# Performance work log

Measured on AMD Instinct MI355X. Metric: run time of the kernel, lower is better.

The kernel has to match this reference:

```python
import jax, jax.numpy as jnp
import numpy as np

B, S, D = 4, 2048, 512
H, HD = 8, 64            # n_heads, head_dim = D // H
E, K, F = 8, 2, 1024     # n_experts, top_k, d_ff
EPS = 1e-6


def setup_inputs() -> dict:
    key = jax.random.key(0)
    ks = jax.random.split(key, 16)
    sd = 0.02
    return {
        "inputs": jax.random.normal(ks[0], (B, S, D), jnp.float32),
        "rms1_w": jnp.ones((D,), jnp.float32),
        "wq": jax.random.normal(ks[1], (D, H, HD), jnp.float32) * sd,
        "bq": jnp.zeros((H, HD), jnp.float32),
        "wk": jax.random.normal(ks[2], (D, H, HD), jnp.float32) * sd,
        "bk": jnp.zeros((H, HD), jnp.float32),
        "wv": jax.random.normal(ks[3], (D, H, HD), jnp.float32) * sd,
        "bv": jnp.zeros((H, HD), jnp.float32),
        "wo": jax.random.normal(ks[4], (H, HD, D), jnp.float32) * sd,
        "bo": jnp.zeros((D,), jnp.float32),
        "rms2_w": jnp.ones((D,), jnp.float32),
        "gate_w": jax.random.normal(ks[5], (D, E), jnp.float32) * sd,
        "ew1": jax.random.normal(ks[6], (E, D, F), jnp.float32) * sd,
        "eb1": jnp.zeros((E, F), jnp.float32),
        "ew2": jax.random.normal(ks[7], (E, F, D), jnp.float32) * sd,
        "eb2": jnp.zeros((E, D), jnp.float32),
    }


def _rmsnorm(x, w):
    return x * jax.lax.rsqrt(jnp.mean(x * x, axis=-1, keepdims=True) + EPS) * w


def _mha(x, wq, bq, wk, bk, wv, bv, wo, bo):
    q = jnp.einsum("bsd,dhe->bshe", x, wq) + bq
    k = jnp.einsum("bsd,dhe->bshe", x, wk) + bk
    v = jnp.einsum("bsd,dhe->bshe", x, wv) + bv
    scores = jnp.einsum("bqhe,bkhe->bhqk", q, k) / jnp.sqrt(jnp.float32(HD))
    attn = jax.nn.softmax(scores, axis=-1)
    ctx = jnp.einsum("bhqk,bkhe->bqhe", attn, v)
    return jnp.einsum("bqhe,hed->bqd", ctx, wo) + bo


def _moe(x, gate_w, ew1, eb1, ew2, eb2):
    T = B * S
    xt = x.reshape(T, D)
    probs = jax.nn.softmax(xt @ gate_w, axis=-1)          # [T, E]
    topv, topi = jax.lax.top_k(probs, K)                   # [T, K]
    topv = topv / jnp.sum(topv, axis=-1, keepdims=True)    # renormalize
    # dense combine weights [T, E]
    wmat = jnp.sum(jax.nn.one_hot(topi, E, dtype=xt.dtype) * topv[..., None], axis=1)
    h = jax.nn.relu(jnp.einsum("td,edf->tef", xt, ew1) + eb1)   # [T, E, F]
    y = jnp.einsum("tef,efd->ted", h, ew2) + eb2                # [T, E, D]
    out = jnp.einsum("te,ted->td", wmat, y)
    return out.reshape(B, S, D)


def reference(inputs, rms1_w, wq, bq, wk, bk, wv, bv, wo, bo, rms2_w, gate_w, ew1, eb1, ew2, eb2):
    x = _rmsnorm(inputs, rms1_w)
    x = _mha(x, wq, bq, wk, bk, wv, bv, wo, bo)
    x1 = x + inputs
    x = _rmsnorm(x1, rms2_w)
    x = _moe(x, gate_w, ew1, eb1, ew2, eb2)
    # dropout is identity at inference
    return x + x1
```

## Files before the change

### kernel.cpp

```cpp
#include <hip/hip_runtime.h>
#include <hip/hip_bf16.h>

typedef unsigned short u16;
typedef __attribute__((ext_vector_type(8))) short short8;
typedef __attribute__((ext_vector_type(4))) short bf16x4;
typedef __attribute__((ext_vector_type(4))) float f32x4;
typedef __attribute__((ext_vector_type(4))) int i32x4;
typedef __attribute__((ext_vector_type(2))) unsigned u32x2;

#define DEV __device__ __forceinline__

DEV float bf2f(u16 v){ unsigned u = ((unsigned)v)<<16; float f; __builtin_memcpy(&f,&u,4); return f; }
DEV u16 f2bf(float f){ unsigned u; __builtin_memcpy(&u,&f,4); u += 0x7fff + ((u>>16)&1); return (u16)(u>>16); }

DEV void gload16(const void* g, void* l){
  __builtin_amdgcn_global_load_lds((const __attribute__((address_space(1))) void*)g,
                                   (__attribute__((address_space(3))) void*)l, 16, 0, 0);
}


__global__ __launch_bounds__(256) void k_tconv(const float* __restrict__ src, u16* __restrict__ dst,
    int R, int C){
  src += (size_t)blockIdx.z * R * C;
  dst += (size_t)blockIdx.z * R * C;
  int r0 = blockIdx.y * 64, c0 = blockIdx.x * 64;
  __shared__ u16 tile[64][68];
  int tid = threadIdx.x;
  int rr = tid >> 4, cc = (tid & 15) * 4;
  #pragma unroll
  for (int it = 0; it < 4; ++it){
    int r = it*16 + rr;
    float4 v = *(const float4*)(src + (size_t)(r0 + r)*C + c0 + cc);
    bf16x4 pk = { (short)f2bf(v.x), (short)f2bf(v.y), (short)f2bf(v.z), (short)f2bf(v.w) };
    *(bf16x4*)&tile[r][cc] = pk;
  }
  __syncthreads();
  #pragma unroll
  for (int it = 0; it < 4; ++it){
    int c = it*16 + rr;
    bf16x4 pk = { (short)tile[cc+0][c], (short)tile[cc+1][c],
                  (short)tile[cc+2][c], (short)tile[cc+3][c] };
    *(bf16x4*)(dst + (size_t)(c0 + c)*R + r0 + cc) = pk;
  }
}

__global__ __launch_bounds__(256) void k_vtrans(const u16* __restrict__ src, u16* __restrict__ dst){
  int bh = blockIdx.y; int s0 = blockIdx.x*64;
  src += (size_t)bh*2048*64 + (size_t)s0*64;
  dst += (size_t)bh*64*2048 + s0;
  __shared__ unsigned tile[64*33];
  int tid = threadIdx.x;
  #pragma unroll
  for (int it = 0; it < 2; ++it){
    int c = tid + it*256;
    int r = c >> 3, c8 = c & 7;
    i32x4 v = *(const i32x4*)(src + (size_t)r*64 + c8*8);
    *(i32x4*)&tile[r*33 + c8*4] = v;
  }
  __syncthreads();
  #pragma unroll
  for (int it = 0; it < 2; ++it){
    int c = tid + it*256;
    int d = c >> 3, s8 = c & 7;
    union { i32x4 v; u16 us[8]; } o;
    #pragma unroll
    for (int j = 0; j < 8; ++j){
      unsigned w = tile[(s8*8+j)*33 + (d>>1)];
      o.us[j] = (d & 1) ? (u16)(w >> 16) : (u16)(w & 0xffff);
    }
    *(i32x4*)(dst + (size_t)d*2048 + s8*8) = o.v;
  }
}

__global__ __launch_bounds__(256) void k_rmsnorm(const float* __restrict__ x, const float* __restrict__ w,
    u16* __restrict__ ob){
  int t = blockIdx.x, tid = threadIdx.x;
  const float* xr = x + (size_t)t*512;
  float2 v = *(const float2*)(xr + tid*2);
  float ss = v.x*v.x + v.y*v.y;
  #pragma unroll
  for (int o=32; o>0; o>>=1) ss += __shfl_down(ss, o);
  __shared__ float sred[4];
  if ((tid&63)==0) sred[tid>>6] = ss;
  __syncthreads();
  float tot = sred[0]+sred[1]+sred[2]+sred[3];
  float inv = rsqrtf(tot*(1.f/512.f) + 1e-6f);
  float2 wv = *(const float2*)(w + tid*2);
  ob[(size_t)t*512 + tid*2]     = f2bf(v.x*inv*wv.x);
  ob[(size_t)t*512 + tid*2 + 1] = f2bf(v.y*inv*wv.y);
}

__global__ __launch_bounds__(256) void k_rmsgate(const float* __restrict__ x, const float* __restrict__ w,
    const float* __restrict__ gw, u16* __restrict__ ob, int* __restrict__ topi, float* __restrict__ topw){
  int t = blockIdx.x, tid = threadIdx.x;
  const float* xr = x + (size_t)t*512;
  float2 v = *(const float2*)(xr + tid*2);
  float ss = v.x*v.x + v.y*v.y;
  #pragma unroll
  for (int o=32; o>0; o>>=1) ss += __shfl_down(ss, o);
  __shared__ float sred[4];
  if ((tid&63)==0) sred[tid>>6] = ss;
  __syncthreads();
  float tot = sred[0]+sred[1]+sred[2]+sred[3];
  float inv = rsqrtf(tot*(1.f/512.f) + 1e-6f);
  float2 wv = *(const float2*)(w + tid*2);
  float y0 = v.x*inv*wv.x, y1 = v.y*inv*wv.y;
  ob[(size_t)t*512 + tid*2]     = f2bf(y0);
  ob[(size_t)t*512 + tid*2 + 1] = f2bf(y1);
  float acc[8];
  const float* g0 = gw + tid*16;
  #pragma unroll
  for (int e=0;e<8;e++) acc[e] = y0*g0[e] + y1*g0[8+e];
  #pragma unroll
  for (int dd=1; dd<64; dd<<=1)
    #pragma unroll
    for (int e=0;e<8;e++) acc[e] += __shfl_xor(acc[e], dd);
  __shared__ float gred[4][8];
  if ((tid&63)==0)
    #pragma unroll
    for (int e=0;e<8;e++) gred[tid>>6][e] = acc[e];
  __syncthreads();
  if (tid==0){
    float l[8];
    #pragma unroll
    for (int e=0;e<8;e++) l[e] = gred[0][e]+gred[1][e]+gred[2][e]+gred[3][e];
    int i0=0; float a0=l[0];
    #pragma unroll
    for (int e=1;e<8;e++) if (l[e]>a0){ a0=l[e]; i0=e; }
    int i1=-1; float a1=-1e30f;
    #pragma unroll
    for (int e=0;e<8;e++) if (e!=i0 && l[e]>a1){ a1=l[e]; i1=e; }
    float w1 = __expf(a1 - a0);
    float invs = 1.f / (1.f + w1);
    topi[t*2]=i0; topi[t*2+1]=i1;
    topw[t*2]=invs; topw[t*2+1]=w1*invs;
  }
}

__global__ __launch_bounds__(256) void k_count(const int* __restrict__ topi, int* __restrict__ counts){
  __shared__ int lcnt[8];
  if (threadIdx.x < 8) lcnt[threadIdx.x] = 0;
  __syncthreads();
  for (int i = blockIdx.x*256 + threadIdx.x; i < 16384; i += 256*64)
    atomicAdd(&lcnt[topi[i]], 1);
  __syncthreads();
  if (threadIdx.x < 8) atomicAdd(&counts[threadIdx.x], lcnt[threadIdx.x]);
}

template<int MODE>
__global__ __launch_bounds__(256) void k_gemm(const u16* __restrict__ A, const u16* __restrict__ Bt,
    int Nsize, int Ksize,
    const float* __restrict__ b0, const float* __restrict__ b1, const float* __restrict__ b2,
    const float* __restrict__ resid, float* __restrict__ outf,
    u16* __restrict__ o0, u16* __restrict__ o1, u16* __restrict__ o2,
    const int* __restrict__ ebase, const int* __restrict__ ecnt, const int* __restrict__ etok)
{
  int nNT = Nsize >> 7;
  int e=0, mt, nt, myBase=0, myCnt=0;
  if constexpr (MODE>=2){
    int per = 128*nNT;
    e = blockIdx.x / per;
    int rr = blockIdx.x - e*per;
    mt = rr / nNT; nt = rr - mt*nNT;
    myCnt = ecnt[e]; myBase = ebase[e];
    if (mt*128 >= myCnt) return;
    Bt += (size_t)e * Nsize * Ksize;
  } else {
    mt = blockIdx.x / nNT; nt = blockIdx.x - mt*nNT;
  }
  __shared__ u16 As[128*32];
  __shared__ u16 Bs[128*32];
  int tid = threadIdx.x;
  int lane = tid & 63, wid = tid >> 6;
  int wr = (wid>>1)<<6, wc = (wid&1)<<6;
  int lrow = lane & 15, lk8 = (lane>>4)<<3;
  const u16* asrc[2]; const u16* bsrc[2];
  u16* aldst[2]; u16* bldst[2];
  #pragma unroll
  for (int it=0; it<2; ++it){
    int c = it*256 + tid;
    int r = c >> 2, c4 = c & 3;
    int grow;
    if constexpr (MODE==2){
      int ml = mt*128 + r; if (ml >= myCnt) ml = myCnt-1;
      grow = etok[myBase + ml];
    } else if constexpr (MODE==3){
      int ml = mt*128 + r; if (ml >= myCnt) ml = myCnt-1;
      grow = myBase + ml;
    } else {
      grow = mt*128 + r;
    }
    asrc[it] = A + (size_t)grow*Ksize + c4*8;
    bsrc[it] = Bt + (size_t)(nt*128 + r)*Ksize + c4*8;
    aldst[it] = As + (it*256 + wid*64)*8;
    bldst[it] = Bs + (it*256 + wid*64)*8;
  }
  f32x4 acc[4][4] = {};
  int nK = Ksize >> 5;
  for (int ks = 0; ks < nK; ++ks){
    int k0 = ks<<5;
    #pragma unroll
    for (int it=0; it<2; ++it){
      gload16(asrc[it] + k0, aldst[it]);
      gload16(bsrc[it] + k0, bldst[it]);
    }
    __syncthreads();
    short8 a[4], b[4];
    #pragma unroll
    for (int i=0;i<4;i++) a[i] = *(const short8*)(As + (wr + i*16 + lrow)*32 + lk8);
    #pragma unroll
    for (int j=0;j<4;j++) b[j] = *(const short8*)(Bs + (wc + j*16 + lrow)*32 + lk8);
    #pragma unroll
    for (int i=0;i<4;i++)
      #pragma unroll
      for (int j=0;j<4;j++)
        acc[i][j] = __builtin_amdgcn_mfma_f32_16x16x32_bf16(a[i], b[j], acc[i][j], 0,0,0);
    __syncthreads();
  }
  #pragma unroll
  for (int i=0;i<4;i++){
    #pragma unroll
    for (int r=0;r<4;r++){
      int rowl = mt*128 + wr + i*16 + ((lane>>4)<<2) + r;
      #pragma unroll
      for (int j=0;j<4;j++){
        int col = nt*128 + wc + j*16 + lrow;
        float v = acc[i][j][r];
        if constexpr (MODE==0){
          int which = col >> 9; int hc = col & 511;
          const float* bias = which==0 ? b0 : (which==1 ? b1 : b2);
          v += bias[hc];
          if (which == 0) v *= 0.18033688011112042f;
          u16* dst = which==0 ? o0 : (which==1 ? o1 : o2);
          int bidx = rowl >> 11, s = rowl & 2047;
          int h = hc >> 6, hd = hc & 63;
          dst[((size_t)(bidx*8+h)*2048 + s)*64 + hd] = f2bf(v);
        } else if constexpr (MODE==1){
          v += b0[col] + resid[(size_t)rowl*512 + col];
          outf[(size_t)rowl*512 + col] = v;
        } else if constexpr (MODE==2){
          if (rowl < myCnt){
            v += b0[e*1024 + col];
            v = fmaxf(v, 0.f);
            o0[(size_t)(myBase+rowl)*1024 + col] = f2bf(v);
          }
        } else {
          if (rowl < myCnt){
            v += b0[e*512 + col];
            o0[(size_t)(myBase+rowl)*512 + col] = f2bf(v);
          }
        }
      }
    }
  }
}

__global__ __launch_bounds__(256) void k_attn(const u16* __restrict__ qb, const u16* __restrict__ kb,
    const u16* __restrict__ vtb, u16* __restrict__ ctx)
{
  int qt = blockIdx.x & 15;
  int bh = blockIdx.x >> 4;
  int b = bh >> 3, h = bh & 7;
  const size_t bho = (size_t)bh * (2048*64);
  int tid = threadIdx.x, lane = tid & 63, wid = tid >> 6;
  int lrow = lane & 15, g = lane >> 4;
  __shared__ u16 Ks[128*64];
  __shared__ u16 Vts[64*128];
  __shared__ u16 Ps[4][32*128];
  char* Ksb = (char*)Ks;
  char* Vsb = (char*)Vts;
  char* Psb = (char*)&Ps[wid][0];
  int q0 = qt*128 + wid*32;
  short8 qf[2][2];
  #pragma unroll
  for (int mm=0;mm<2;mm++)
    #pragma unroll
    for (int kf=0;kf<2;kf++)
      qf[mm][kf] = *(const short8*)(qb + bho + (size_t)(q0 + mm*16 + lrow)*64 + kf*32 + g*8);
  f32x4 oacc[2][4] = {};
  float lpart[2] = {0.f, 0.f};
  const int swz = (lrow & 7) << 4;

  size_t ksrc[4], vsrc[4];
  int kdst[4], vdst[4];
  #pragma unroll
  for (int it=0; it<4; ++it){
    int c = tid + it*256;
    int kr = c >> 3, kc8 = c & 7;
    ksrc[it] = bho + (size_t)kr*64 + kc8*8;
    kdst[it] = kr*128 + ((kc8*16) ^ ((kr&7)<<4));
    int vr = c >> 4, vc16 = c & 15;
    vsrc[it] = bho + (size_t)vr*2048 + vc16*8;
    vdst[it] = vr*256 + ((vc16*16) ^ ((vr&7)<<4));
  }
  i32x4 kreg[4], vreg[4];
  #pragma unroll
  for (int it=0; it<4; ++it){
    kreg[it] = *(const i32x4*)(kb + ksrc[it]);
    vreg[it] = *(const i32x4*)(vtb + vsrc[it]);
  }
  #pragma unroll
  for (int it=0; it<4; ++it){
    *(i32x4*)(Ksb + kdst[it]) = kreg[it];
    *(i32x4*)(Vsb + vdst[it]) = vreg[it];
  }
  __syncthreads();

  for (int kt=0; kt<16; ++kt){
    if (kt < 15){
      int k0 = (kt+1)*128;
      #pragma unroll
      for (int it=0; it<4; ++it){
        kreg[it] = *(const i32x4*)(kb + ksrc[it] + (size_t)k0*64);
        vreg[it] = *(const i32x4*)(vtb + vsrc[it] + k0);
      }
    }
    __builtin_amdgcn_s_setprio(1);
    #pragma unroll
    for (int nf=0; nf<8; ++nf){
      short8 kf0 = *(const short8*)(Ksb + (nf*16+lrow)*128 + ((g*16) ^ swz));
      short8 kf1 = *(const short8*)(Ksb + (nf*16+lrow)*128 + ((64 + g*16) ^ swz));
      #pragma unroll
      for (int mm=0; mm<2; ++mm){
        f32x4 s = {};
        s = __builtin_amdgcn_mfma_f32_16x16x32_bf16(kf0, qf[mm][0], s, 0,0,0);
        s = __builtin_amdgcn_mfma_f32_16x16x32_bf16(kf1, qf[mm][1], s, 0,0,0);
        float p0 = __builtin_amdgcn_exp2f(s[0]);
        float p1 = __builtin_amdgcn_exp2f(s[1]);
        float p2 = __builtin_amdgcn_exp2f(s[2]);
        float p3 = __builtin_amdgcn_exp2f(s[3]);
        lpart[mm] += (p0+p1)+(p2+p3);
        unsigned w0 = (unsigned)f2bf(p0) | ((unsigned)f2bf(p1)<<16);
        unsigned w1 = (unsigned)f2bf(p2) | ((unsigned)f2bf(p3)<<16);
        *(u32x2*)(Psb + (mm*16+lrow)*256 + ((nf*32 + g*8) ^ swz)) = (u32x2){w0, w1};
      }
    }
    short8 pfr[2][4];
    #pragma unroll
    for (int mm=0;mm<2;mm++)
      #pragma unroll
      for (int kf=0;kf<4;kf++)
        pfr[mm][kf] = *(const short8*)(Psb + (mm*16+lrow)*256 + ((kf*64 + g*16) ^ swz));
    #pragma unroll
    for (int dn=0;dn<4;dn++){
      #pragma unroll
      for (int kf=0;kf<4;kf++){
        short8 vf = *(const short8*)(Vsb + (dn*16+lrow)*256 + ((kf*64 + g*16) ^ swz));
        #pragma unroll
        for (int mm=0;mm<2;mm++)
          oacc[mm][dn] = __builtin_amdgcn_mfma_f32_16x16x32_bf16(pfr[mm][kf], vf, oacc[mm][dn], 0,0,0);
      }
    }
    __builtin_amdgcn_s_setprio(0);
    __syncthreads();
    if (kt < 15){
      #pragma unroll
      for (int it=0; it<4; ++it){
        *(i32x4*)(Ksb + kdst[it]) = kreg[it];
        *(i32x4*)(Vsb + vdst[it]) = vreg[it];
      }
      __syncthreads();
    }
  }
  float linv[2][4];
  #pragma unroll
  for (int mm=0;mm<2;mm++){
    float ls = lpart[mm];
    ls += __shfl_xor(ls, 16);
    ls += __shfl_xor(ls, 32);
    #pragma unroll
    for (int r=0;r<4;r++)
      linv[mm][r] = 1.0f / __shfl(ls, g*4 + r);
  }
  #pragma unroll
  for (int mm=0;mm<2;mm++){
    #pragma unroll
    for (int r=0;r<4;r++){
      int qrow = q0 + mm*16 + g*4 + r;
      #pragma unroll
      for (int dn=0;dn<4;dn++)
        ctx[((size_t)(b*2048 + qrow))*512 + h*64 + dn*16 + lrow] = f2bf(oacc[mm][dn][r] * linv[mm][r]);
    }
  }
}

__global__ void k_scan(const int* __restrict__ counts, int* __restrict__ base, int* __restrict__ cur){
  if (threadIdx.x==0 && blockIdx.x==0){
    int s=0;
    for (int e=0;e<8;e++){ base[e]=s; cur[e]=s; s+=counts[e]; }
  }
}

__global__ __launch_bounds__(256) void k_assign(const int* __restrict__ topi,
    int* __restrict__ cur, int* __restrict__ rowof, int* __restrict__ tokof)
{
  __shared__ int lcnt[8];
  __shared__ int gbase[8];
  int tid = threadIdx.x;
  if (tid < 8) lcnt[tid] = 0;
  __syncthreads();
  int t = blockIdx.x*256 + tid;
  int e0 = topi[t*2], e1 = topi[t*2+1];
  int r0 = atomicAdd(&lcnt[e0], 1);
  int r1 = atomicAdd(&lcnt[e1], 1);
  __syncthreads();
  if (tid < 8) gbase[tid] = atomicAdd(&cur[tid], lcnt[tid]);
  __syncthreads();
  int row0 = gbase[e0] + r0, row1 = gbase[e1] + r1;
  rowof[t*2]   = row0;  rowof[t*2+1] = row1;
  tokof[row0] = t;      tokof[row1] = t;
}

__global__ __launch_bounds__(256) void k_combine(const float* __restrict__ x1, const u16* __restrict__ y,
    const int* __restrict__ rowof, const float* __restrict__ topw, float* __restrict__ out)
{
  int t = blockIdx.x;
  int d0 = threadIdx.x*2;
  int r0 = rowof[t*2], r1 = rowof[t*2+1];
  float w0 = topw[t*2], w1 = topw[t*2+1];
  size_t o = (size_t)t*512 + d0;
  out[o]   = x1[o]   + w0*bf2f(y[(size_t)r0*512+d0])   + w1*bf2f(y[(size_t)r1*512+d0]);
  out[o+1] = x1[o+1] + w0*bf2f(y[(size_t)r0*512+d0+1]) + w1*bf2f(y[(size_t)r1*512+d0+1]);
}

extern "C" void kernel_launch(void* const* d_in, const int* in_sizes, int n_in,
                              void* d_out, int out_size, void* d_ws, size_t ws_size,
                              hipStream_t stream)
{
  const float* inputs = (const float*)d_in[0];
  const float* rms1_w = (const float*)d_in[1];
  const float* wq  = (const float*)d_in[2];
  const float* bq  = (const float*)d_in[3];
  const float* wk  = (const float*)d_in[4];
  const float* bk  = (const float*)d_in[5];
  const float* wv  = (const float*)d_in[6];
  const float* bv  = (const float*)d_in[7];
  const float* wo  = (const float*)d_in[8];
  const float* bo  = (const float*)d_in[9];
  const float* rms2_w = (const float*)d_in[10];
  const float* gate_w = (const float*)d_in[11];
  const float* ew1 = (const float*)d_in[12];
  const float* eb1 = (const float*)d_in[13];
  const float* ew2 = (const float*)d_in[14];
  const float* eb2 = (const float*)d_in[15];
  char* ws = (char*)d_ws;

  size_t off = 0;
  u16* WQKV = (u16*)(ws + off); off += 1536ull*512*2;
  u16* WOT  = (u16*)(ws + off); off += 512ull*512*2;
  u16* E1T  = (u16*)(ws + off); off += 8ull*1024*512*2;
  u16* E2T  = (u16*)(ws + off); off += 8ull*512*1024*2;
  u16* XN   = (u16*)(ws + off); u16* Hbuf = XN;      off += 8192ull*512*2;
  u16* Qb   = (u16*)(ws + off); off += 4ull*8*2048*64*2;
  u16* Kb   = (u16*)(ws + off); off += 4ull*8*2048*64*2;
  u16* Vb   = (u16*)(ws + off); off += 4ull*8*2048*64*2;
  u16* CTX  = (u16*)(ws + off); u16* Yb = CTX;       off += 8192ull*512*2;
  float* XN2F = (float*)(ws + off); u16* VbT = (u16*)XN2F; off += 8192ull*512*4;
  float* X1   = (float*)(ws + off); off += 8192ull*512*4;
  u16* XN2B   = (u16*)(ws + off); off += 8192ull*512*2;
  int*   TOPI = (int*)(ws + off); off += 16384*4;
  float* TOPW = (float*)(ws + off); off += 16384*4;
  int*  ROWOF = (int*)(ws + off); off += 16384*4;
  int*  TOKOF = (int*)(ws + off); off += 16384*4;
  int*  CNT   = (int*)(ws + off); off += 64;
  int*  BASE  = (int*)(ws + off); off += 64;
  int*  CUR   = (int*)(ws + off); off += 64;
  if (ws_size < off) return;
  (void)XN2F;

  k_tconv<<<dim3(8,8,1),   256, 0, stream>>>(wq, WQKV,              512, 512);
  k_tconv<<<dim3(8,8,1),   256, 0, stream>>>(wk, WQKV + 512*512,    512, 512);
  k_tconv<<<dim3(8,8,1),   256, 0, stream>>>(wv, WQKV + 2*512*512,  512, 512);
  k_tconv<<<dim3(8,8,1),   256, 0, stream>>>(wo, WOT,               512, 512);
  k_tconv<<<dim3(16,8,8),  256, 0, stream>>>(ew1, E1T,              512, 1024);
  k_tconv<<<dim3(8,16,8),  256, 0, stream>>>(ew2, E2T,              1024, 512);

  k_rmsnorm<<<8192, 256, 0, stream>>>(inputs, rms1_w, XN);

  k_gemm<0><<<64*12, 256, 0, stream>>>(XN, WQKV, 1536, 512, bq, bk, bv,
      nullptr, nullptr, Qb, Kb, Vb, nullptr, nullptr, nullptr);

  k_vtrans<<<dim3(32,32), 256, 0, stream>>>(Vb, VbT);

  k_attn<<<512, 256, 0, stream>>>(Qb, Kb, VbT, CTX);

  k_gemm<1><<<64*4, 256, 0, stream>>>(CTX, WOT, 512, 512, bo, nullptr, nullptr,
      inputs, X1, nullptr, nullptr, nullptr, nullptr, nullptr, nullptr);

  k_rmsgate<<<8192, 256, 0, stream>>>(X1, rms2_w, gate_w, XN2B, TOPI, TOPW);

  hipMemsetAsync(CNT, 0, 192, stream);
  k_count<<<64, 256, 0, stream>>>(TOPI, CNT);
  k_scan<<<1, 64, 0, stream>>>(CNT, BASE, CUR);
  k_assign<<<32, 256, 0, stream>>>(TOPI, CUR, ROWOF, TOKOF);

  k_gemm<2><<<8*128*8, 256, 0, stream>>>(XN2B, E1T, 1024, 512, eb1, nullptr, nullptr,
      nullptr, nullptr, Hbuf, nullptr, nullptr, BASE, CNT, TOKOF);
  k_gemm<3><<<8*128*4, 256, 0, stream>>>(Hbuf, E2T, 512, 1024, eb2, nullptr, nullptr,
      nullptr, nullptr, Yb, nullptr, nullptr, BASE, CNT, TOKOF);

  k_combine<<<8192, 256, 0, stream>>>(X1, Yb, ROWOF, TOPW, (float*)d_out);
}
```

Before: 269.9 us.

## Double-buffer GEMM LDS tiles and halve attention query tile per block

The bf16 GEMM now uses two LDS buffers for the A and B tiles. It prefetches the next K-slice with global_load_lds while the current slice feeds the MFMAs, removing the load-then-barrier stall at the top of each iteration. The attention kernel drops from 128 to 64 query rows per block, 16 per wave, which doubles the grid to 1024 blocks and shrinks the per-wave P scratch and accumulators. This trades more K/V reloads from global memory for more parallelism and lower register and LDS pressure per block. The GEMM doubles its LDS footprint, which may reduce occupancy.

Result: slower. 275.5 us (+2.1%).

```diff
diff --git a/kernel.cpp b/kernel.cpp
--- a/kernel.cpp
+++ b/kernel.cpp
@@ -168,14 +168,14 @@
   } else {
     mt = blockIdx.x / nNT; nt = blockIdx.x - mt*nNT;
   }
-  __shared__ u16 As[128*32];
-  __shared__ u16 Bs[128*32];
+  __shared__ u16 As[2][128*32];
+  __shared__ u16 Bs[2][128*32];
   int tid = threadIdx.x;
   int lane = tid & 63, wid = tid >> 6;
   int wr = (wid>>1)<<6, wc = (wid&1)<<6;
   int lrow = lane & 15, lk8 = (lane>>4)<<3;
   const u16* asrc[2]; const u16* bsrc[2];
-  u16* aldst[2]; u16* bldst[2];
+  int ldoff[2];
   #pragma unroll
   for (int it=0; it<2; ++it){
     int c = it*256 + tid;
@@ -192,24 +192,31 @@
     }
     asrc[it] = A + (size_t)grow*Ksize + c4*8;
     bsrc[it] = Bt + (size_t)(nt*128 + r)*Ksize + c4*8;
-    aldst[it] = As + (it*256 + wid*64)*8;
-    bldst[it] = Bs + (it*256 + wid*64)*8;
+    ldoff[it] = (it*256 + wid*64)*8;
   }
   f32x4 acc[4][4] = {};
   int nK = Ksize >> 5;
+  #pragma unroll
+  for (int it=0; it<2; ++it){
+    gload16(asrc[it], &As[0][ldoff[it]]);
+    gload16(bsrc[it], &Bs[0][ldoff[it]]);
+  }
+  __syncthreads();
   for (int ks = 0; ks < nK; ++ks){
-    int k0 = ks<<5;
-    #pragma unroll
-    for (int it=0; it<2; ++it){
-      gload16(asrc[it] + k0, aldst[it]);
-      gload16(bsrc[it] + k0, bldst[it]);
-    }
-    __syncthreads();
+    int cur = ks & 1;
+    if (ks+1 < nK){
+      int k0 = (ks+1) << 5;
+      #pragma unroll
+      for (int it=0; it<2; ++it){
+        gload16(asrc[it] + k0, &As[cur^1][ldoff[it]]);
+        gload16(bsrc[it] + k0, &Bs[cur^1][ldoff[it]]);
+      }
+    }
     short8 a[4], b[4];
     #pragma unroll
-    for (int i=0;i<4;i++) a[i] = *(const short8*)(As + (wr + i*16 + lrow)*32 + lk8);
-    #pragma unroll
-    for (int j=0;j<4;j++) b[j] = *(const short8*)(Bs + (wc + j*16 + lrow)*32 + lk8);
+    for (int i=0;i<4;i++) a[i] = *(const short8*)(&As[cur][(wr + i*16 + lrow)*32 + lk8]);
+    #pragma unroll
+    for (int j=0;j<4;j++) b[j] = *(const short8*)(&Bs[cur][(wc + j*16 + lrow)*32 + lk8]);
     #pragma unroll
     for (int i=0;i<4;i++)
       #pragma unroll
@@ -258,27 +265,25 @@
 __global__ __launch_bounds__(256) void k_attn(const u16* __restrict__ qb, const u16* __restrict__ kb,
     const u16* __restrict__ vtb, u16* __restrict__ ctx)
 {
-  int qt = blockIdx.x & 15;
-  int bh = blockIdx.x >> 4;
+  int qt = blockIdx.x & 31;
+  int bh = blockIdx.x >> 5;
   int b = bh >> 3, h = bh & 7;
   const size_t bho = (size_t)bh * (2048*64);
   int tid = threadIdx.x, lane = tid & 63, wid = tid >> 6;
   int lrow = lane & 15, g = lane >> 4;
   __shared__ u16 Ks[128*64];
   __shared__ u16 Vts[64*128];
-  __shared__ u16 Ps[4][32*128];
+  __shared__ u16 Ps[4][16*64];
   char* Ksb = (char*)Ks;
   char* Vsb = (char*)Vts;
   char* Psb = (char*)&Ps[wid][0];
-  int q0 = qt*128 + wid*32;
-  short8 qf[2][2];
-  #pragma unroll
-  for (int mm=0;mm<2;mm++)
-    #pragma unroll
-    for (int kf=0;kf<2;kf++)
-      qf[mm][kf] = *(const short8*)(qb + bho + (size_t)(q0 + mm*16 + lrow)*64 + kf*32 + g*8);
-  f32x4 oacc[2][4] = {};
-  float lpart[2] = {0.f, 0.f};
+  int q0 = qt*64 + wid*16;
+  short8 qf[2];
+  #pragma unroll
+  for (int kf=0;kf<2;kf++)
+    qf[kf] = *(const short8*)(qb + bho + (size_t)(q0 + lrow)*64 + kf*32 + g*8);
+  f32x4 oacc[4] = {};
+  float lpart = 0.f;
   const int swz = (lrow & 7) << 4;
 
   size_t ksrc[4], vsrc[4];
@@ -317,38 +322,35 @@
     }
     __builtin_amdgcn_s_setprio(1);
     #pragma unroll
-    for (int nf=0; nf<8; ++nf){
-      short8 kf0 = *(const short8*)(Ksb + (nf*16+lrow)*128 + ((g*16) ^ swz));
-      short8 kf1 = *(const short8*)(Ksb + (nf*16+lrow)*128 + ((64 + g*16) ^ swz));
-      #pragma unroll
-      for (int mm=0; mm<2; ++mm){
+    for (int hf=0; hf<2; ++hf){
+      #pragma unroll
+      for (int nf=0; nf<4; ++nf){
+        int krow = hf*64 + nf*16 + lrow;
+        short8 kf0 = *(const short8*)(Ksb + krow*128 + ((g*16) ^ swz));
+        short8 kf1 = *(const short8*)(Ksb + krow*128 + ((64 + g*16) ^ swz));
         f32x4 s = {};
-        s = __builtin_amdgcn_mfma_f32_16x16x32_bf16(kf0, qf[mm][0], s, 0,0,0);
-        s = __builtin_amdgcn_mfma_f32_16x16x32_bf16(kf1, qf[mm][1], s, 0,0,0);
+        s = __builtin_amdgcn_mfma_f32_16x16x32_bf16(kf0, qf[0], s, 0,0,0);
+        s = __builtin_amdgcn_mfma_f32_16x16x32_bf16(kf1, qf[1], s, 0,0,0);
         float p0 = __builtin_amdgcn_exp2f(s[0]);
         float p1 = __builtin_amdgcn_exp2f(s[1]);
         float p2 = __builtin_amdgcn_exp2f(s[2]);
         float p3 = __builtin_amdgcn_exp2f(s[3]);
-        lpart[mm] += (p0+p1)+(p2+p3);
+        lpart += (p0+p1)+(p2+p3);
         unsigned w0 = (unsigned)f2bf(p0) | ((unsigned)f2bf(p1)<<16);
         unsigned w1 = (unsigned)f2bf(p2) | ((unsigned)f2bf(p3)<<16);
-        *(u32x2*)(Psb + (mm*16+lrow)*256 + ((nf*32 + g*8) ^ swz)) = (u32x2){w0, w1};
-      }
-    }
-    short8 pfr[2][4];
-    #pragma unroll
-    for (int mm=0;mm<2;mm++)
-      #pragma unroll
-      for (int kf=0;kf<4;kf++)
-        pfr[mm][kf] = *(const short8*)(Psb + (mm*16+lrow)*256 + ((kf*64 + g*16) ^ swz));
-    #pragma unroll
-    for (int dn=0;dn<4;dn++){
-      #pragma unroll
-      for (int kf=0;kf<4;kf++){
-        short8 vf = *(const short8*)(Vsb + (dn*16+lrow)*256 + ((kf*64 + g*16) ^ swz));
+        *(u32x2*)(Psb + lrow*128 + ((nf*32 + g*8) ^ swz)) = (u32x2){w0, w1};
+      }
+      short8 pfr[2];
+      #pragma unroll
+      for (int kf=0;kf<2;kf++)
+        pfr[kf] = *(const short8*)(Psb + lrow*128 + ((kf*64 + g*16) ^ swz));
+      #pragma unroll
+      for (int dn=0;dn<4;dn++){
         #pragma unroll
-        for (int mm=0;mm<2;mm++)
-          oacc[mm][dn] = __builtin_amdgcn_mfma_f32_16x16x32_bf16(pfr[mm][kf], vf, oacc[mm][dn], 0,0,0);
+        for (int kf=0;kf<2;kf++){
+          short8 vf = *(const short8*)(Vsb + (dn*16+lrow)*256 + ((hf*128 + kf*64 + g*16) ^ swz));
+          oacc[dn] = __builtin_amdgcn_mfma_f32_16x16x32_bf16(pfr[kf], vf, oacc[dn], 0,0,0);
+        }
       }
     }
     __builtin_amdgcn_s_setprio(0);
@@ -362,25 +364,19 @@
       __syncthreads();
     }
   }
-  float linv[2][4];
-  #pragma unroll
-  for (int mm=0;mm<2;mm++){
-    float ls = lpart[mm];
-    ls += __shfl_xor(ls, 16);
-    ls += __shfl_xor(ls, 32);
-    #pragma unroll
-    for (int r=0;r<4;r++)
-      linv[mm][r] = 1.0f / __shfl(ls, g*4 + r);
-  }
-  #pragma unroll
-  for (int mm=0;mm<2;mm++){
-    #pragma unroll
-    for (int r=0;r<4;r++){
-      int qrow = q0 + mm*16 + g*4 + r;
-      #pragma unroll
-      for (int dn=0;dn<4;dn++)
-        ctx[((size_t)(b*2048 + qrow))*512 + h*64 + dn*16 + lrow] = f2bf(oacc[mm][dn][r] * linv[mm][r]);
-    }
+  float ls = lpart;
+  ls += __shfl_xor(ls, 16);
+  ls += __shfl_xor(ls, 32);
+  float linv[4];
+  #pragma unroll
+  for (int r=0;r<4;r++)
+    linv[r] = 1.0f / __shfl(ls, g*4 + r);
+  #pragma unroll
+  for (int r=0;r<4;r++){
+    int qrow = q0 + g*4 + r;
+    #pragma unroll
+    for (int dn=0;dn<4;dn++)
+      ctx[((size_t)(b*2048 + qrow))*512 + h*64 + dn*16 + lrow] = f2bf(oacc[dn][r] * linv[r]);
   }
 }
 
@@ -482,7 +478,7 @@
 
   k_vtrans<<<dim3(32,32), 256, 0, stream>>>(Vb, VbT);
 
-  k_attn<<<512, 256, 0, stream>>>(Qb, Kb, VbT, CTX);
+  k_attn<<<1024, 256, 0, stream>>>(Qb, Kb, VbT, CTX);
 
   k_gemm<1><<<64*4, 256, 0, stream>>>(CTX, WOT, 512, 512, bo, nullptr, nullptr,
       inputs, X1, nullptr, nullptr, nullptr, nullptr, nullptr, nullptr);
```
